# Kernel tuning notes

Hardware: AMD Instinct MI355X
Metric: run time of the kernel (lower is better)

## Reference

```python
import jax, jax.numpy as jnp
import numpy as np


def setup_inputs() -> dict:
    key = jax.random.key(0)
    k1, k2, k3, k4 = jax.random.split(key, 4)
    N, Cin, H, W = 4, 32, 64, 64
    Cout, K = 64, 3
    fan = Cin * K * K
    x = jax.random.normal(k1, (N, Cin, H, W), jnp.float32)
    # kaiming_normal init for AEG weight; standard conv init for the dense conv
    weight = jax.random.normal(k2, (Cout, Cin, K, K), jnp.float32) * np.float32(np.sqrt(2.0 / fan))
    conv_w = jax.random.normal(k3, (Cout, Cin, K, K), jnp.float32) * np.float32(np.sqrt(1.0 / fan))
    conv_b = jax.random.normal(k4, (Cout,), jnp.float32) * np.float32(0.01)
    return {"x": x, "weight": weight, "conv_w": conv_w, "conv_b": conv_b}


def _aeg_conv(x, weight, stride, padding):
    # Faithful translation of conv2d_aeg_optimized, but the per-tap recurrence
    # runs under lax.scan and never materializes the (N,Cout,Cin,K2,L) tensor.
    N, Cin, H, W = x.shape
    Cout, _, KH, KW = weight.shape
    xp = jnp.pad(x, ((0, 0), (0, 0), (padding, padding), (padding, padding)))
    oh = (H - KH + 2 * padding) // stride + 1
    ow = (W - KW + 2 * padding) // stride + 1
    # per-tap shifted views of the padded input: (K2, N, Cin, oh, ow)
    taps = jnp.stack([
        xp[:, :, ki:ki + (oh - 1) * stride + 1:stride, kj:kj + (ow - 1) * stride + 1:stride]
        for ki in range(KH) for kj in range(KW)
    ])
    kflat = weight.reshape(Cout, Cin, KH * KW).transpose(2, 0, 1)  # (K2, Cout, Cin)
    # mask[k, i, j] = (i + j + k) % 2 == 0 where i = l // ow, j = l % ow
    ii = jnp.arange(oh)[:, None]
    jj = jnp.arange(ow)[None, :]
    kk = jnp.arange(KH * KW)[:, None, None]
    mask = (ii + jj + kk) % 2 == 0  # (K2, oh, ow)

    def step(res, tap):
        xk, yk, mk = tap
        xk = xk[:, None]                      # (N, 1, Cin, oh, ow)
        yk = yk[None, :, :, None, None]       # (1, Cout, Cin, 1, 1)
        mk = mk[None, None, None]             # (1, 1, 1, oh, ow)
        res = jnp.where(mk, (res + xk) * yk, (res + yk) * xk)
        return res, None

    res0 = jnp.zeros((N, Cout, Cin, oh, ow), x.dtype)
    res, _ = jax.lax.scan(step, res0, (taps, kflat, mask))
    return res.sum(axis=2)  # (N, Cout, oh, ow)


def reference(x, weight, conv_w, conv_b):
    stride, padding = 1, 1
    aeg = _aeg_conv(x, weight, stride, padding)
    conv = jax.lax.conv_general_dilated(
        x, conv_w, window_strides=(stride, stride),
        padding=[(padding, padding), (padding, padding)],
        dimension_numbers=("NCHW", "OIHW", "NCHW"),
    ) + conv_b[None, :, None, None]
    return jax.nn.sigmoid(aeg) * conv
```

## Files before the change

kernel.cpp:

```cpp
#include <hip/hip_runtime.h>

#define CIN   32
#define COUT  64
#define HH    64
#define WW    64
#define NB    4
#define TH    8
#define HR    (TH + 2)
#define G     8
#define CPT   2
#define ROWCI 72

__device__ __forceinline__ float2 pk_fma_(float2 a, float2 b, float2 c) {
    float2 d;
    asm("v_pk_fma_f32 %0, %1, %2, %3" : "=v"(d) : "v"(a), "v"(b), "v"(c));
    return d;
}
__device__ __forceinline__ float2 pk_add_(float2 a, float2 b) {
    float2 d;
    asm("v_pk_add_f32 %0, %1, %2" : "=v"(d) : "v"(a), "v"(b));
    return d;
}
template<int HI>
__device__ __forceinline__ float2 pk_mul_sel(float2 a, float2 b) {
    float2 d;
    if (HI) asm("v_pk_mul_f32 %0, %1, %2 op_sel:[0,1] op_sel_hi:[1,1]" : "=v"(d) : "v"(a), "v"(b));
    else    asm("v_pk_mul_f32 %0, %1, %2 op_sel:[0,0] op_sel_hi:[1,0]" : "=v"(d) : "v"(a), "v"(b));
    return d;
}
template<int HI>
__device__ __forceinline__ float2 pk_fma_sel(float2 a, float2 b, float2 c) {
    float2 d;
    if (HI) asm("v_pk_fma_f32 %0, %1, %2, %3 op_sel:[0,1,0] op_sel_hi:[1,1,1]" : "=v"(d) : "v"(a), "v"(b), "v"(c));
    else    asm("v_pk_fma_f32 %0, %1, %2, %3 op_sel:[0,0,0] op_sel_hi:[1,0,1]" : "=v"(d) : "v"(a), "v"(b), "v"(c));
    return d;
}

template<int S>
__device__ __forceinline__ void math_g(const float* __restrict__ sx,
                                       const float* __restrict__ sw,
                                       int lrow, int m, int cb, int g,
                                       float2 aeg2[CPT], float2 cv2[CPT])
{
    #pragma unroll 2
    for (int cl = 0; cl < G; ++cl) {
        const int ci = g + cl;
        float tc[5], tl[5], tr[5];
        #pragma unroll
        for (int wr = 0; wr < 5; ++wr) {
            const int qc = (wr & 1) ^ 1 ^ S;
            const float* rowp = sx + (lrow + wr) * (G * ROWCI) + cl * ROWCI;
            tc[wr] = rowp[qc * 36 + 1 + m];
            const float* sp = rowp + (1 - qc) * 36 + m + cb;
            tl[wr] = sp[0];
            tr[wr] = sp[1];
        }
        float2 t2c[3], t2l[3], t2r[3];
        #pragma unroll
        for (int wr = 0; wr < 3; ++wr) {
            t2c[wr] = make_float2(tc[wr], tc[wr + 2]);
            t2l[wr] = make_float2(tl[wr], tl[wr + 2]);
            t2r[wr] = make_float2(tr[wr], tr[wr + 2]);
        }

        float w[36];
        const float* pw = sw + ci * 36;
        #pragma unroll
        for (int u = 0; u < 9; ++u)
            *(float4*)&w[4 * u] = *(const float4*)&pw[4 * u];
        const float2* w2 = (const float2*)w;

        #pragma unroll
        for (int c = 0; c < CPT; ++c) {
            float2 r2 = make_float2(0.0f, 0.0f);
            #pragma unroll
            for (int k = 0; k < 9; ++k) {
                const int wr = k / 3;
                const int kj = k % 3;
                const float2 t2 = (kj == 0) ? t2l[wr] : ((kj == 1) ? t2c[wr] : t2r[wr]);
                const int ia = c * 9 + k;
                const int ic = 18 + c * 9 + k;
                float2 prod = (ia & 1) ? pk_mul_sel<1>(t2, w2[ia / 2])
                                       : pk_mul_sel<0>(t2, w2[ia / 2]);
                if ((k & 1) == S)
                    r2 = (ia & 1) ? pk_fma_sel<1>(r2, w2[ia / 2], prod)
                                  : pk_fma_sel<0>(r2, w2[ia / 2], prod);
                else
                    r2 = pk_fma_(r2, t2, prod);
                cv2[c] = (ic & 1) ? pk_fma_sel<1>(t2, w2[ic / 2], cv2[c])
                                  : pk_fma_sel<0>(t2, w2[ic / 2], cv2[c]);
            }
            aeg2[c] = pk_add_(aeg2[c], r2);
        }
    }
}

__global__ __launch_bounds__(256, 4)
void aeg_conv_kernel(const float* __restrict__ x,
                     const float* __restrict__ weight,
                     const float* __restrict__ conv_w,
                     const float* __restrict__ conv_b,
                     float* __restrict__ out)
{
    __shared__ float sx[HR * G * ROWCI];
    __shared__ float sw[CIN * 36];

    const int tid = threadIdx.x;
    const int i0  = blockIdx.x * TH;
    const int n   = blockIdx.y;
    const int co0 = blockIdx.z * CPT;

    const int s  = (tid >> 6) & 1;
    const int rg = tid >> 7;
    const int h  = (tid >> 5) & 1;
    const int m  = tid & 31;

    const int rb_local = rg * 4 + h;
    const int rb  = i0 + rb_local;
    const int cb  = (rb & 1) ^ s;
    const int col = 2 * m + cb;

    const float* xn = x + (size_t)n * (CIN * HH * WW);

    for (int idx = tid; idx < HR * G * 2 * 2; idx += 256) {
        int arr  = idx >> 1;
        int slot = (idx & 1) ? 33 : 0;
        sx[arr * 36 + slot] = 0.0f;
    }

    for (int idx = tid; idx < CIN * 36; idx += 256) {
        int ci = idx / 36, slot = idx - ci * 36;
        int set = slot / 18, rem = slot - set * 18;
        int c2 = rem / 9, k = rem - c2 * 9;
        const float* src = set ? conv_w : weight;
        sw[idx] = src[((size_t)(co0 + c2) * CIN + ci) * 9 + k];
    }

    float2 aeg2[CPT], cv2[CPT];
    #pragma unroll
    for (int c = 0; c < CPT; ++c) {
        aeg2[c] = make_float2(0.0f, 0.0f);
        cv2[c]  = make_float2(0.0f, 0.0f);
    }

    for (int g = 0; g < CIN; g += G) {
        __syncthreads();
        #pragma unroll
        for (int it = 0; it < 5; ++it) {
            int idx  = it * 256 + tid;
            int f4   = idx & 15;
            int pair = idx >> 4;
            int r10  = pair >> 3;
            int cl   = pair & 7;
            int gi   = i0 - 1 + r10;
            float4 v = make_float4(0.f, 0.f, 0.f, 0.f);
            if ((unsigned)gi < (unsigned)HH)
                v = *(const float4*)&xn[(g + cl) * (HH * WW) + gi * WW + 4 * f4];
            int rp   = gi & 1;
            float* base = &sx[pair * ROWCI];
            base[rp * 36 + 1 + 2 * f4]        = v.x;
            base[rp * 36 + 2 + 2 * f4]        = v.z;
            base[(rp ^ 1) * 36 + 1 + 2 * f4]  = v.y;
            base[(rp ^ 1) * 36 + 2 + 2 * f4]  = v.w;
        }
        __syncthreads();

        if (s == 0) math_g<0>(sx, sw, rb_local, m, cb, g, aeg2, cv2);
        else        math_g<1>(sx, sw, rb_local, m, cb, g, aeg2, cv2);
    }

    #pragma unroll
    for (int p = 0; p < 2; ++p) {
        int i = rb + 2 * p;
        #pragma unroll
        for (int c = 0; c < CPT; ++c) {
            int co = co0 + c;
            float a = p ? aeg2[c].y : aeg2[c].x;
            float v = p ? cv2[c].y  : cv2[c].x;
            float conv = v + conv_b[co];
            float sg = 1.0f / (1.0f + __expf(-a));
            out[(((size_t)n * COUT + co) * HH + i) * WW + col] = sg * conv;
        }
    }
}

extern "C" void kernel_launch(void* const* d_in, const int* in_sizes, int n_in,
                              void* d_out, int out_size, void* d_ws, size_t ws_size,
                              hipStream_t stream) {
    const float* x      = (const float*)d_in[0];
    const float* weight = (const float*)d_in[1];
    const float* conv_w = (const float*)d_in[2];
    const float* conv_b = (const float*)d_in[3];
    float* out = (float*)d_out;

    dim3 grid(HH / TH, NB, COUT / CPT);
    aeg_conv_kernel<<<grid, 256, 0, stream>>>(x, weight, conv_w, conv_b, out);
}
```

Baseline: 33.54 us.

## Compute one output channel per block with smaller channel groups for higher occupancy

Each block now computes a single output channel instead of two, with input-channel group size halved and weights packed to 20 floats per channel. The launch bound is raised to target 8 blocks per CU, and the grid doubles along the output-channel axis. The intent is lower register and LDS pressure and more parallelism. The cost is halved reuse of each loaded input tile, so input loads and LDS reads per FLOP double.

```diff
diff --git a/kernel.cpp b/kernel.cpp
--- a/kernel.cpp
+++ b/kernel.cpp
@@ -7,9 +7,9 @@
 #define NB    4
 #define TH    8
 #define HR    (TH + 2)
-#define G     8
-#define CPT   2
+#define G     4
 #define ROWCI 72
+#define WPK   20
 
 __device__ __forceinline__ float2 pk_fma_(float2 a, float2 b, float2 c) {
     float2 d;
@@ -40,7 +40,7 @@
 __device__ __forceinline__ void math_g(const float* __restrict__ sx,
                                        const float* __restrict__ sw,
                                        int lrow, int m, int cb, int g,
-                                       float2 aeg2[CPT], float2 cv2[CPT])
+                                       float2& aeg2, float2& cv2)
 {
     #pragma unroll 2
     for (int cl = 0; cl < G; ++cl) {
@@ -63,39 +63,36 @@
             t2r[wr] = make_float2(tr[wr], tr[wr + 2]);
         }
 
-        float w[36];
-        const float* pw = sw + ci * 36;
+        float w[WPK];
+        const float* pw = sw + ci * WPK;
         #pragma unroll
-        for (int u = 0; u < 9; ++u)
+        for (int u = 0; u < 5; ++u)
             *(float4*)&w[4 * u] = *(const float4*)&pw[4 * u];
         const float2* w2 = (const float2*)w;
 
+        float2 r2 = make_float2(0.0f, 0.0f);
         #pragma unroll
-        for (int c = 0; c < CPT; ++c) {
-            float2 r2 = make_float2(0.0f, 0.0f);
-            #pragma unroll
-            for (int k = 0; k < 9; ++k) {
-                const int wr = k / 3;
-                const int kj = k % 3;
-                const float2 t2 = (kj == 0) ? t2l[wr] : ((kj == 1) ? t2c[wr] : t2r[wr]);
-                const int ia = c * 9 + k;
-                const int ic = 18 + c * 9 + k;
-                float2 prod = (ia & 1) ? pk_mul_sel<1>(t2, w2[ia / 2])
-                                       : pk_mul_sel<0>(t2, w2[ia / 2]);
-                if ((k & 1) == S)
-                    r2 = (ia & 1) ? pk_fma_sel<1>(r2, w2[ia / 2], prod)
-                                  : pk_fma_sel<0>(r2, w2[ia / 2], prod);
-                else
-                    r2 = pk_fma_(r2, t2, prod);
-                cv2[c] = (ic & 1) ? pk_fma_sel<1>(t2, w2[ic / 2], cv2[c])
-                                  : pk_fma_sel<0>(t2, w2[ic / 2], cv2[c]);
-            }
-            aeg2[c] = pk_add_(aeg2[c], r2);
+        for (int k = 0; k < 9; ++k) {
+            const int wr = k / 3;
+            const int kj = k % 3;
+            const float2 t2 = (kj == 0) ? t2l[wr] : ((kj == 1) ? t2c[wr] : t2r[wr]);
+            const int ia = k;
+            const int ic = 10 + k;
+            float2 prod = (ia & 1) ? pk_mul_sel<1>(t2, w2[ia / 2])
+                                   : pk_mul_sel<0>(t2, w2[ia / 2]);
+            if ((k & 1) == S)
+                r2 = (ia & 1) ? pk_fma_sel<1>(r2, w2[ia / 2], prod)
+                              : pk_fma_sel<0>(r2, w2[ia / 2], prod);
+            else
+                r2 = pk_fma_(r2, t2, prod);
+            cv2 = (ic & 1) ? pk_fma_sel<1>(t2, w2[ic / 2], cv2)
+                           : pk_fma_sel<0>(t2, w2[ic / 2], cv2);
         }
+        aeg2 = pk_add_(aeg2, r2);
     }
 }
 
-__global__ __launch_bounds__(256, 4)
+__global__ __launch_bounds__(256, 8)
 void aeg_conv_kernel(const float* __restrict__ x,
                      const float* __restrict__ weight,
                      const float* __restrict__ conv_w,
@@ -103,12 +100,12 @@
                      float* __restrict__ out)
 {
     __shared__ float sx[HR * G * ROWCI];
-    __shared__ float sw[CIN * 36];
+    __shared__ float sw[CIN * WPK];
 
     const int tid = threadIdx.x;
     const int i0  = blockIdx.x * TH;
     const int n   = blockIdx.y;
-    const int co0 = blockIdx.z * CPT;
+    const int co  = blockIdx.z;
 
     const int s  = (tid >> 6) & 1;
     const int rg = tid >> 7;
@@ -128,40 +125,38 @@
         sx[arr * 36 + slot] = 0.0f;
     }
 
-    for (int idx = tid; idx < CIN * 36; idx += 256) {
-        int ci = idx / 36, slot = idx - ci * 36;
-        int set = slot / 18, rem = slot - set * 18;
-        int c2 = rem / 9, k = rem - c2 * 9;
-        const float* src = set ? conv_w : weight;
-        sw[idx] = src[((size_t)(co0 + c2) * CIN + ci) * 9 + k];
+    for (int idx = tid; idx < CIN * WPK; idx += 256) {
+        int ci = idx / WPK, slot = idx - ci * WPK;
+        float v = 0.0f;
+        if (slot < 9)                    v = weight[((size_t)co * CIN + ci) * 9 + slot];
+        else if (slot >= 10 && slot < 19) v = conv_w[((size_t)co * CIN + ci) * 9 + (slot - 10)];
+        sw[idx] = v;
     }
 
-    float2 aeg2[CPT], cv2[CPT];
-    #pragma unroll
-    for (int c = 0; c < CPT; ++c) {
-        aeg2[c] = make_float2(0.0f, 0.0f);
-        cv2[c]  = make_float2(0.0f, 0.0f);
-    }
+    float2 aeg2 = make_float2(0.0f, 0.0f);
+    float2 cv2  = make_float2(0.0f, 0.0f);
 
     for (int g = 0; g < CIN; g += G) {
         __syncthreads();
         #pragma unroll
-        for (int it = 0; it < 5; ++it) {
-            int idx  = it * 256 + tid;
-            int f4   = idx & 15;
-            int pair = idx >> 4;
-            int r10  = pair >> 3;
-            int cl   = pair & 7;
-            int gi   = i0 - 1 + r10;
-            float4 v = make_float4(0.f, 0.f, 0.f, 0.f);
-            if ((unsigned)gi < (unsigned)HH)
-                v = *(const float4*)&xn[(g + cl) * (HH * WW) + gi * WW + 4 * f4];
-            int rp   = gi & 1;
-            float* base = &sx[pair * ROWCI];
-            base[rp * 36 + 1 + 2 * f4]        = v.x;
-            base[rp * 36 + 2 + 2 * f4]        = v.z;
-            base[(rp ^ 1) * 36 + 1 + 2 * f4]  = v.y;
-            base[(rp ^ 1) * 36 + 2 + 2 * f4]  = v.w;
+        for (int it = 0; it < 3; ++it) {
+            int idx = it * 256 + tid;
+            if (idx < HR * G * 16) {
+                int f4   = idx & 15;
+                int pair = idx >> 4;
+                int r10  = pair >> 2;
+                int cl   = pair & 3;
+                int gi   = i0 - 1 + r10;
+                float4 v = make_float4(0.f, 0.f, 0.f, 0.f);
+                if ((unsigned)gi < (unsigned)HH)
+                    v = *(const float4*)&xn[(g + cl) * (HH * WW) + gi * WW + 4 * f4];
+                int rp   = gi & 1;
+                float* base = &sx[pair * ROWCI];
+                base[rp * 36 + 1 + 2 * f4]        = v.x;
+                base[rp * 36 + 2 + 2 * f4]        = v.z;
+                base[(rp ^ 1) * 36 + 1 + 2 * f4]  = v.y;
+                base[(rp ^ 1) * 36 + 2 + 2 * f4]  = v.w;
+            }
         }
         __syncthreads();
 
@@ -169,18 +164,15 @@
         else        math_g<1>(sx, sw, rb_local, m, cb, g, aeg2, cv2);
     }
 
+    const float bias = conv_b[co];
     #pragma unroll
     for (int p = 0; p < 2; ++p) {
         int i = rb + 2 * p;
-        #pragma unroll
-        for (int c = 0; c < CPT; ++c) {
-            int co = co0 + c;
-            float a = p ? aeg2[c].y : aeg2[c].x;
-            float v = p ? cv2[c].y  : cv2[c].x;
-            float conv = v + conv_b[co];
-            float sg = 1.0f / (1.0f + __expf(-a));
-            out[(((size_t)n * COUT + co) * HH + i) * WW + col] = sg * conv;
-        }
+        float a = p ? aeg2.y : aeg2.x;
+        float v = p ? cv2.y  : cv2.x;
+        float conv = v + bias;
+        float sg = 1.0f / (1.0f + __expf(-a));
+        out[(((size_t)n * COUT + co) * HH + i) * WW + col] = sg * conv;
     }
 }
 
@@ -193,6 +185,6 @@
     const float* conv_b = (const float*)d_in[3];
     float* out = (float*)d_out;
 
-    dim3 grid(HH / TH, NB, COUT / CPT);
+    dim3 grid(HH / TH, NB, COUT);
     aeg_conv_kernel<<<grid, 256, 0, stream>>>(x, weight, conv_w, conv_b, out);
 }
```

Result: slower. 44.07 us (+31.4%).
